# Performance work log

Hardware: AMD Instinct MI355X
Metric: run time of the kernel (lower is better)

## Reference

```python
import jax, jax.numpy as jnp
import numpy as np

EPS = 1e-5

def _conv1x1(x, w, b):
    # x: [B,C,...], w: [O,C], b: [O]
    y = jnp.einsum('oc,bc...->bo...', w, x)
    return y + b.reshape((1, -1) + (1,) * (x.ndim - 2))

def _bn(x, g, be, m, v):
    # inference-mode BatchNorm with running stats (PyTorch eps=1e-5)
    s = (1, -1) + (1,) * (x.ndim - 2)
    return (x - m.reshape(s)) * (g.reshape(s) / jnp.sqrt(v.reshape(s) + EPS)) + be.reshape(s)

def _patches3x3(x):
    # F.unfold(kernel=3, pad=1, stride=1, dil=1): [B,C,H,W] -> [B,C,9,H,W], row-major kernel order
    B, C, H, W = x.shape
    xp = jnp.pad(x, ((0, 0), (0, 0), (1, 1), (1, 1)))
    return jnp.stack([xp[:, :, ky:ky + H, kx:kx + W] for ky in range(3) for kx in range(3)], axis=2)

def setup_inputs() -> dict:
    key = jax.random.key(0)
    ks = jax.random.split(key, 40)
    B, Cin, H, W = 4, 16, 192, 192
    Cm = 64  # mlp[-1]
    d = {}
    d['x'] = jax.random.normal(ks[0], (B, Cin, H, W), jnp.float32)
    d['group_mask'] = jnp.ones((B, 1, H, W), jnp.float32)
    d['group_xyz'] = jax.random.normal(ks[1], (B, 3, 9, H, W), jnp.float32)
    def bnp(k, c):
        k1, k2, k3, k4 = jax.random.split(k, 4)
        return (1.0 + 0.1 * jax.random.normal(k1, (c,)), 0.1 * jax.random.normal(k2, (c,)),
                0.1 * jax.random.normal(k3, (c,)), 0.5 + jax.random.uniform(k4, (c,)))
    d['w0'] = 0.1 * jax.random.normal(ks[2], (Cm, Cin)); d['b0'] = 0.01 * jax.random.normal(ks[3], (Cm,))
    d['g0'], d['beta0'], d['m0'], d['v0'] = bnp(ks[4], Cm)
    wn_dims = [(8, 3), (8, 8), (16, 8)]
    for i, (o, c) in enumerate(wn_dims):
        d[f'wn_w{i}'] = 0.3 * jax.random.normal(ks[5 + 3 * i], (o, c))
        d[f'wn_b{i}'] = 0.01 * jax.random.normal(ks[6 + 3 * i], (o,))
        d[f'wn_g{i}'], d[f'wn_beta{i}'], d[f'wn_m{i}'], d[f'wn_v{i}'] = bnp(ks[7 + 3 * i], o)
    d['lw'] = 0.05 * jax.random.normal(ks[20], (Cm, 16 * Cm)); d['lb'] = 0.01 * jax.random.normal(ks[21], (Cm,))
    d['lg'], d['lbeta'], d['lm'], d['lv'] = bnp(ks[22], Cm)
    return d

def reference(x, group_mask, group_xyz,
              w0, b0, g0, beta0, m0, v0,
              wn_w0, wn_b0, wn_g0, wn_beta0, wn_m0, wn_v0,
              wn_w1, wn_b1, wn_g1, wn_beta1, wn_m1, wn_v1,
              wn_w2, wn_b2, wn_g2, wn_beta2, wn_m2, wn_v2,
              lw, lb, lg, lbeta, lm, lv):
    # mlp_convs chain (single layer here)
    x = jax.nn.relu(_bn(_conv1x1(x, w0, b0), g0, beta0, m0, v0))  # [B,Cm,H,W]
    B, _, N, H, W = group_xyz.shape
    # WeightNet on local coords: [B,3,N,H*W] -> [B,16,N,H*W]
    gz = group_xyz.reshape(B, 3, N, H * W)
    for w, b, g, be, m, v in ((wn_w0, wn_b0, wn_g0, wn_beta0, wn_m0, wn_v0),
                              (wn_w1, wn_b1, wn_g1, wn_beta1, wn_m1, wn_v1),
                              (wn_w2, wn_b2, wn_g2, wn_beta2, wn_m2, wn_v2)):
        gz = jax.nn.relu(_bn(_conv1x1(gz, w, b), g, be, m, v))
    gz = gz.reshape(B, 16, N, H, W)
    p = _patches3x3(x)  # [B,Cm,9,H,W]
    C = p.shape[1]
    # per-pixel matmul: [B,H,W,C,9] @ [B,H,W,9,16] -> [B,H,W,C,16]
    out = jnp.einsum('bckhw,bokhw->bhwco', p, gz)
    out = out.reshape(B, H, W, C * 16).transpose(0, 3, 1, 2)  # [B,16*Cm,H,W]
    return jax.nn.relu(_bn(_conv1x1(out, lw, lb), lg, lbeta, lm, lv))
```

## Files before the change

### kernel.cpp

```cpp
#include <hip/hip_runtime.h>
#include <hip/hip_bf16.h>

#define HH 192
#define WW 192
#define HWPROD (192*192)
#define EPSBN 1e-5f

typedef _Float16 f16x8 __attribute__((ext_vector_type(8)));
typedef _Float16 f16x4 __attribute__((ext_vector_type(4)));
typedef _Float16 f16x2 __attribute__((ext_vector_type(2)));
typedef float f32x4 __attribute__((ext_vector_type(4)));

__global__ __launch_bounds__(256) void prep_conv0_k(
                       const float* __restrict__ w0, const float* __restrict__ b0,
                       const float* __restrict__ g0, const float* __restrict__ beta0,
                       const float* __restrict__ m0, const float* __restrict__ v0,
                       const float* __restrict__ wnw0, const float* __restrict__ wnb0,
                       const float* __restrict__ wng0, const float* __restrict__ wnbe0,
                       const float* __restrict__ wnm0, const float* __restrict__ wnv0,
                       const float* __restrict__ wnw1, const float* __restrict__ wnb1,
                       const float* __restrict__ wng1, const float* __restrict__ wnbe1,
                       const float* __restrict__ wnm1, const float* __restrict__ wnv1,
                       const float* __restrict__ wnw2, const float* __restrict__ wnb2,
                       const float* __restrict__ wng2, const float* __restrict__ wnbe2,
                       const float* __restrict__ wnm2, const float* __restrict__ wnv2,
                       const float* __restrict__ lw, const float* __restrict__ lb,
                       const float* __restrict__ lg, const float* __restrict__ lbeta,
                       const float* __restrict__ lm, const float* __restrict__ lv,
                       const float* __restrict__ x,
                       _Float16* __restrict__ x1L,
                       _Float16* __restrict__ whF,
                       float* __restrict__ lbf,
                       float* __restrict__ wnP)
{
    const int tid = threadIdx.x;

    if (blockIdx.x >= 576) {
        int idx = (blockIdx.x - 576) * 256 + tid;
        if (idx < 65536) {
            int j    = idx & 7;
            int lane = (idx >> 3) & 63;
            int kg   = (idx >> 9) & 31;
            int nt   = idx >> 14;
            int k = kg * 32 + ((lane >> 4) & 3) * 8 + j;
            int n = nt * 16 + (lane & 15);
            float s = lg[n] * rsqrtf(lv[n] + EPSBN);
            whF[idx] = (_Float16)(lw[n * 1024 + k] * s);
        } else if (idx < 65600) {
            int j = idx - 65536;
            float s = lg[j] * rsqrtf(lv[j] + EPSBN);
            lbf[j] = (lb[j] - lm[j]) * s + lbeta[j];
        } else if (idx < 65848) {
            int t = idx - 65600;
            if (t < 24)       { int o = t / 3;           float s = wng0[o] * rsqrtf(wnv0[o] + EPSBN); wnP[t] = wnw0[t] * s; }
            else if (t < 32)  { int o = t - 24;          float s = wng0[o] * rsqrtf(wnv0[o] + EPSBN); wnP[t] = (wnb0[o] - wnm0[o]) * s + wnbe0[o]; }
            else if (t < 96)  { int t2 = t - 32;  int o = t2 >> 3; float s = wng1[o] * rsqrtf(wnv1[o] + EPSBN); wnP[t] = wnw1[t2] * s; }
            else if (t < 104) { int o = t - 96;          float s = wng1[o] * rsqrtf(wnv1[o] + EPSBN); wnP[t] = (wnb1[o] - wnm1[o]) * s + wnbe1[o]; }
            else if (t < 232) { int t2 = t - 104; int o = t2 >> 3; float s = wng2[o] * rsqrtf(wnv2[o] + EPSBN); wnP[t] = wnw2[t2] * s; }
            else if (t < 248) { int o = t - 232;         float s = wng2[o] * rsqrtf(wnv2[o] + EPSBN); wnP[t] = (wnb2[o] - wnm2[o]) * s + wnbe2[o]; }
        }
        return;
    }

    __shared__ float wSt[16][64];
    __shared__ float bS[64];
    for (int t = tid; t < 1024; t += 256) {
        int o = t >> 4, ci = t & 15;
        float s = g0[o] * rsqrtf(v0[o] + EPSBN);
        wSt[ci][o] = w0[t] * s;
    }
    if (tid < 64) {
        float s = g0[tid] * rsqrtf(v0[tid] + EPSBN);
        bS[tid] = (b0[tid] - m0[tid]) * s + beta0[tid];
    }
    __syncthreads();

    const int pix = blockIdx.x * 256 + tid;
    const int b = pix / HWPROD;
    const int p = pix - b * HWPROD;

    float xv[16];
#pragma unroll
    for (int cin = 0; cin < 16; cin++)
        xv[cin] = x[((size_t)b * 16 + cin) * HWPROD + p];

    _Float16* outp = x1L + (size_t)pix * 64;
#pragma unroll
    for (int co = 0; co < 64; co += 4) {
        f32x4 a = { bS[co], bS[co + 1], bS[co + 2], bS[co + 3] };
#pragma unroll
        for (int cin = 0; cin < 16; cin++) {
            float xc = xv[cin];
            a.x += wSt[cin][co + 0] * xc;
            a.y += wSt[cin][co + 1] * xc;
            a.z += wSt[cin][co + 2] * xc;
            a.w += wSt[cin][co + 3] * xc;
        }
        a.x = fmaxf(a.x, 0.f); a.y = fmaxf(a.y, 0.f);
        a.z = fmaxf(a.z, 0.f); a.w = fmaxf(a.w, 0.f);
        *(f16x4*)(outp + co) = __builtin_convertvector(a, f16x4);
    }
}

__global__ __launch_bounds__(512, 4) void pconv_main_k(const float* __restrict__ gxyz,
                                                       const _Float16* __restrict__ x1L,
                                                       const _Float16* __restrict__ whF,
                                                       const float* __restrict__ lbf,
                                                       const float* __restrict__ wnP,
                                                       float* __restrict__ out)
{
    __shared__ __align__(16) char smem[58496];
    f16x2*    xtP = reinterpret_cast<f16x2*>(smem);
    _Float16* A0  = reinterpret_cast<_Float16*>(smem + 25728);
    _Float16* A1  = reinterpret_cast<_Float16*>(smem + 42112);
    _Float16* gzF = reinterpret_cast<_Float16*>(smem + 25728);
    float*    Cb  = reinterpret_cast<float*>(smem);

    const int tid = threadIdx.x;
    const int bid = blockIdx.x;
    const int b   = bid / (HH * 3);
    const int rem = bid % (HH * 3);
    const int h   = rem / 3;
    const int wc0 = (rem % 3) * 64;

    for (int q = tid; q < 1584; q += 512) {
        int c8   = q & 7;
        int colr = q >> 3;
        int col  = colr % 66;
        int r    = colr / 66;
        int hr = h + r - 1;
        int wc = wc0 + col - 1;
        union { f16x8 v; f16x2 p[4]; } U;
        U.v = f16x8{};
        if (hr >= 0 && hr < HH && wc >= 0 && wc < WW) {
            U.v = *(const f16x8*)(x1L + (((size_t)b * HH + hr) * WW + wc) * 64 + c8 * 8);
        }
#pragma unroll
        for (int i = 0; i < 4; i++)
            xtP[(c8 * 4 + i) * 201 + colr] = U.p[i];
    }

    for (int u = tid; u < 576; u += 512) {
        int pixu = u & 63, tap = u >> 6;
        size_t base = ((size_t)(b * 3) * 9 + tap) * HWPROD + (size_t)h * WW + wc0 + pixu;
        float z0 = gxyz[base];
        float z1 = gxyz[base + (size_t)9 * HWPROD];
        float z2 = gxyz[base + (size_t)18 * HWPROD];
        float h0[8], h1[8];
#pragma unroll
        for (int o = 0; o < 8; o++) {
            float a = wnP[24 + o] + wnP[o * 3 + 0] * z0 + wnP[o * 3 + 1] * z1 + wnP[o * 3 + 2] * z2;
            h0[o] = fmaxf(a, 0.f);
        }
#pragma unroll
        for (int o = 0; o < 8; o++) {
            float a = wnP[96 + o];
#pragma unroll
            for (int c = 0; c < 8; c++) a += wnP[32 + o * 8 + c] * h0[c];
            h1[o] = fmaxf(a, 0.f);
        }
        float g[16];
#pragma unroll
        for (int o = 0; o < 16; o++) {
            float a = wnP[232 + o];
#pragma unroll
            for (int c = 0; c < 8; c++) a += wnP[104 + o * 8 + c] * h1[c];
            g[o] = fmaxf(a, 0.f);
        }
        f16x8 lo, hi;
#pragma unroll
        for (int o = 0; o < 8; o++) { lo[o] = (_Float16)g[o]; hi[o] = (_Float16)g[o + 8]; }
        *(f16x8*)&gzF[pixu * 152 + tap * 16]     = lo;
        *(f16x8*)&gzF[pixu * 152 + tap * 16 + 8] = hi;
    }
    __syncthreads();

    const int pix = tid & 63;
    const int u8  = tid >> 6;
    const int oh  = u8 & 1;
    const int cp  = u8 >> 1;
    const int lane = tid & 63;
    const int wv   = tid >> 6;
    const int nt   = wv & 3;
    const int mt2  = wv >> 2;

    f16x2 gq2[9][4];
#pragma unroll
    for (int t = 0; t < 9; t++) {
        union { f16x8 v; f16x2 h[4]; } G;
        G.v = *(const f16x8*)&gzF[pix * 152 + t * 16 + oh * 8];
#pragma unroll
        for (int d = 0; d < 4; d++) gq2[t][d] = G.h[d];
    }
    __syncthreads();

    const int mt = pix >> 4;

    auto phase1 = [&](int cc, _Float16* Ab) {
        union { f16x2 h2[4]; f16x8 v; } av0, av1;
#pragma unroll
        for (int d = 0; d < 4; d++) { av0.h2[d] = f16x2{0, 0}; av1.h2[d] = f16x2{0, 0}; }
        const f16x2* xrow = xtP + (cc * 4 + cp) * 201 + pix;
#pragma unroll
        for (int ky = 0; ky < 3; ky++) {
#pragma unroll
            for (int kx = 0; kx < 3; kx++) {
                const int t = ky * 3 + kx;
                f16x2 xq = xrow[ky * 66 + kx];
                f16x2 xb0 = __builtin_shufflevector(xq, xq, 0, 0);
                f16x2 xb1 = __builtin_shufflevector(xq, xq, 1, 1);
#pragma unroll
                for (int d = 0; d < 4; d++) {
                    av0.h2[d] = __builtin_elementwise_fma(xb0, gq2[t][d], av0.h2[d]);
                    av1.h2[d] = __builtin_elementwise_fma(xb1, gq2[t][d], av1.h2[d]);
                }
            }
        }
        const int row = cp * 4 + mt;
        *(f16x8*)&Ab[(row * 64 + (pix & 15) + 16 * oh) * 8]       = av0.v;
        *(f16x8*)&Ab[(row * 64 + (pix & 15) + 16 * (2 + oh)) * 8] = av1.v;
    };

    const f16x8* whF8 = (const f16x8*)whF;
    f32x4 facc[2];
    facc[0] = f32x4{0.f, 0.f, 0.f, 0.f};
    facc[1] = f32x4{0.f, 0.f, 0.f, 0.f};

    phase1(0, A0);
    __syncthreads();

#pragma unroll 2
    for (int cc = 0; cc < 8; cc++) {
        const _Float16* Ac = (cc & 1) ? A1 : A0;
#pragma unroll
        for (int kb = 0; kb < 4; kb++) {
            const int kg = cc * 4 + kb;
            f16x8 a0 = *(const f16x8*)&Ac[((kb * 4 + 2 * mt2) * 64 + lane) * 8];
            f16x8 a1 = *(const f16x8*)&Ac[((kb * 4 + 2 * mt2 + 1) * 64 + lane) * 8];
            f16x8 wh = whF8[((nt * 32 + kg) << 6) + lane];
            facc[0] = __builtin_amdgcn_mfma_f32_16x16x32_f16(a0, wh, facc[0], 0, 0, 0);
            facc[1] = __builtin_amdgcn_mfma_f32_16x16x32_f16(a1, wh, facc[1], 0, 0, 0);
        }
        if (cc < 7) phase1(cc + 1, (cc & 1) ? A0 : A1);
        __syncthreads();
    }

    {
        const int n = nt * 16 + (lane & 15);
        const float bias = lbf[n];
#pragma unroll
        for (int m = 0; m < 2; m++) {
            const int pixm = (2 * mt2 + m) * 16 + (lane >> 4) * 4;
#pragma unroll
            for (int r = 0; r < 4; r++)
                Cb[n * 67 + pixm + r] = fmaxf(facc[m][r] + bias, 0.f);
        }
    }
    __syncthreads();
    {
        const int pixq = tid & 63, jq = tid >> 6;
        size_t ob = ((size_t)b * 64 + jq * 8) * HWPROD + (size_t)h * WW + wc0 + pixq;
#pragma unroll
        for (int i = 0; i < 8; i++) {
            out[ob + (size_t)i * HWPROD] = Cb[(jq * 8 + i) * 67 + pixq];
        }
    }
}

extern "C" void kernel_launch(void* const* d_in, const int* in_sizes, int n_in,
                              void* d_out, int out_size, void* d_ws, size_t ws_size,
                              hipStream_t stream) {
    const float* x    = (const float*)d_in[0];
    const float* gxyz = (const float*)d_in[2];

    char* ws = (char*)d_ws;
    _Float16* x1L = (_Float16*)ws;
    _Float16* whF = x1L + 9437184;
    float* lbf = (float*)(whF + 65536);
    float* wnP = lbf + 64;

    prep_conv0_k<<<838, 256, 0, stream>>>(
        (const float*)d_in[3],  (const float*)d_in[4],  (const float*)d_in[5],
        (const float*)d_in[6],  (const float*)d_in[7],  (const float*)d_in[8],
        (const float*)d_in[9],  (const float*)d_in[10], (const float*)d_in[11],
        (const float*)d_in[12], (const float*)d_in[13], (const float*)d_in[14],
        (const float*)d_in[15], (const float*)d_in[16], (const float*)d_in[17],
        (const float*)d_in[18], (const float*)d_in[19], (const float*)d_in[20],
        (const float*)d_in[21], (const float*)d_in[22], (const float*)d_in[23],
        (const float*)d_in[24], (const float*)d_in[25], (const float*)d_in[26],
        (const float*)d_in[27], (const float*)d_in[28], (const float*)d_in[29],
        (const float*)d_in[30], (const float*)d_in[31], (const float*)d_in[32],
        x, x1L, whF, lbf, wnP);

    pconv_main_k<<<4 * HH * 3, 512, 0, stream>>>(gxyz, x1L, whF, lbf, wnP,
                                                 (float*)d_out);
}
```

Before: 221.4 us.

## Halve A-tile double buffers to raise occupancy from 4 to 6 blocks

Each phase1 step now builds half as many channels: one scalar channel per thread instead of an f16x2 pair. The K loop therefore runs 16 half-chunks of 2 MFMA k-blocks instead of 8 chunks of 4. This shrinks each A staging buffer by half, which cuts LDS to 45184 bytes, and the launch bounds are raised to 6 blocks per CU so more waves can hide latency. In exchange there are twice as many __syncthreads barriers. It also adds scalar half loads from LDS and lowers the per-thread ILP inside phase1.

```diff
diff --git a/kernel.cpp b/kernel.cpp
--- a/kernel.cpp
+++ b/kernel.cpp
@@ -102,17 +102,17 @@
     }
 }
 
-__global__ __launch_bounds__(512, 4) void pconv_main_k(const float* __restrict__ gxyz,
+__global__ __launch_bounds__(512, 6) void pconv_main_k(const float* __restrict__ gxyz,
                                                        const _Float16* __restrict__ x1L,
                                                        const _Float16* __restrict__ whF,
                                                        const float* __restrict__ lbf,
                                                        const float* __restrict__ wnP,
                                                        float* __restrict__ out)
 {
-    __shared__ __align__(16) char smem[58496];
+    __shared__ __align__(16) char smem[45184];
     f16x2*    xtP = reinterpret_cast<f16x2*>(smem);
     _Float16* A0  = reinterpret_cast<_Float16*>(smem + 25728);
-    _Float16* A1  = reinterpret_cast<_Float16*>(smem + 42112);
+    _Float16* A1  = reinterpret_cast<_Float16*>(smem + 33920);
     _Float16* gzF = reinterpret_cast<_Float16*>(smem + 25728);
     float*    Cb  = reinterpret_cast<float*>(smem);
 
@@ -178,7 +178,7 @@
     const int pix = tid & 63;
     const int u8  = tid >> 6;
     const int oh  = u8 & 1;
-    const int cp  = u8 >> 1;
+    const int cw  = u8 >> 1;
     const int lane = tid & 63;
     const int wv   = tid >> 6;
     const int nt   = wv & 3;
@@ -195,30 +195,27 @@
     __syncthreads();
 
     const int mt = pix >> 4;
-
-    auto phase1 = [&](int cc, _Float16* Ab) {
-        union { f16x2 h2[4]; f16x8 v; } av0, av1;
-#pragma unroll
-        for (int d = 0; d < 4; d++) { av0.h2[d] = f16x2{0, 0}; av1.h2[d] = f16x2{0, 0}; }
-        const f16x2* xrow = xtP + (cc * 4 + cp) * 201 + pix;
+    const _Float16* xtH = reinterpret_cast<const _Float16*>(smem);
+
+    auto phase1 = [&](int hc, _Float16* Ab) {
+        union { f16x2 h2[4]; f16x8 v; } av;
+#pragma unroll
+        for (int d = 0; d < 4; d++) av.h2[d] = f16x2{0, 0};
+        const _Float16* xrow = xtH + (size_t)((hc * 2 + (cw >> 1)) * 201 + pix) * 2 + (cw & 1);
 #pragma unroll
         for (int ky = 0; ky < 3; ky++) {
 #pragma unroll
             for (int kx = 0; kx < 3; kx++) {
                 const int t = ky * 3 + kx;
-                f16x2 xq = xrow[ky * 66 + kx];
-                f16x2 xb0 = __builtin_shufflevector(xq, xq, 0, 0);
-                f16x2 xb1 = __builtin_shufflevector(xq, xq, 1, 1);
-#pragma unroll
-                for (int d = 0; d < 4; d++) {
-                    av0.h2[d] = __builtin_elementwise_fma(xb0, gq2[t][d], av0.h2[d]);
-                    av1.h2[d] = __builtin_elementwise_fma(xb1, gq2[t][d], av1.h2[d]);
-                }
+                _Float16 xs = xrow[(ky * 66 + kx) * 2];
+                f16x2 xb = { xs, xs };
+#pragma unroll
+                for (int d = 0; d < 4; d++)
+                    av.h2[d] = __builtin_elementwise_fma(xb, gq2[t][d], av.h2[d]);
             }
         }
-        const int row = cp * 4 + mt;
-        *(f16x8*)&Ab[(row * 64 + (pix & 15) + 16 * oh) * 8]       = av0.v;
-        *(f16x8*)&Ab[(row * 64 + (pix & 15) + 16 * (2 + oh)) * 8] = av1.v;
+        const int row = (cw >> 1) * 4 + mt;
+        *(f16x8*)&Ab[(row * 64 + (pix & 15) + 16 * ((cw & 1) * 2 + oh)) * 8] = av.v;
     };
 
     const f16x8* whF8 = (const f16x8*)whF;
@@ -230,18 +227,18 @@
     __syncthreads();
 
 #pragma unroll 2
-    for (int cc = 0; cc < 8; cc++) {
-        const _Float16* Ac = (cc & 1) ? A1 : A0;
-#pragma unroll
-        for (int kb = 0; kb < 4; kb++) {
-            const int kg = cc * 4 + kb;
+    for (int hc = 0; hc < 16; hc++) {
+        const _Float16* Ac = (hc & 1) ? A1 : A0;
+#pragma unroll
+        for (int kb = 0; kb < 2; kb++) {
+            const int kg = hc * 2 + kb;
             f16x8 a0 = *(const f16x8*)&Ac[((kb * 4 + 2 * mt2) * 64 + lane) * 8];
             f16x8 a1 = *(const f16x8*)&Ac[((kb * 4 + 2 * mt2 + 1) * 64 + lane) * 8];
             f16x8 wh = whF8[((nt * 32 + kg) << 6) + lane];
             facc[0] = __builtin_amdgcn_mfma_f32_16x16x32_f16(a0, wh, facc[0], 0, 0, 0);
             facc[1] = __builtin_amdgcn_mfma_f32_16x16x32_f16(a1, wh, facc[1], 0, 0, 0);
         }
-        if (cc < 7) phase1(cc + 1, (cc & 1) ? A0 : A1);
+        if (hc < 15) phase1(hc + 1, (hc & 1) ? A0 : A1);
         __syncthreads();
     }
 
```

New measurement: 223.2 us. About the same (+0.8%).

## Switch final GEMM to 32x32x16 MFMA with split-K across wave halves

Applied to the files above, without the earlier changes.

The final 1x1 conv GEMM now uses 32x32x16 MFMA tiles instead of pairs of 16x16x32, with the weight pre-layout and A-tile layout reorganized to match. The eight waves split K by alternating channel chunks: half the waves process even chunks and half odd chunks, then combine partial sums through shared memory before bias and ReLU. This aims to cut the number of MFMA issues and LDS/global weight loads per wave. In exchange it adds a shared-memory reduction step and leaves half of the waves idle during each chunk's MFMA phase.

```diff
diff --git a/kernel.cpp b/kernel.cpp
--- a/kernel.cpp
+++ b/kernel.cpp
@@ -10,6 +10,7 @@
 typedef _Float16 f16x4 __attribute__((ext_vector_type(4)));
 typedef _Float16 f16x2 __attribute__((ext_vector_type(2)));
 typedef float f32x4 __attribute__((ext_vector_type(4)));
+typedef float f32x16 __attribute__((ext_vector_type(16)));
 
 __global__ __launch_bounds__(256) void prep_conv0_k(
                        const float* __restrict__ w0, const float* __restrict__ b0,
@@ -40,10 +41,10 @@
         if (idx < 65536) {
             int j    = idx & 7;
             int lane = (idx >> 3) & 63;
-            int kg   = (idx >> 9) & 31;
-            int nt   = idx >> 14;
-            int k = kg * 32 + ((lane >> 4) & 3) * 8 + j;
-            int n = nt * 16 + (lane & 15);
+            int kg   = (idx >> 9) & 63;
+            int nt   = idx >> 15;
+            int k = kg * 16 + ((lane >> 5) & 1) * 8 + j;
+            int n = nt * 32 + (lane & 31);
             float s = lg[n] * rsqrtf(lv[n] + EPSBN);
             whF[idx] = (_Float16)(lw[n * 1024 + k] * s);
         } else if (idx < 65600) {
@@ -115,6 +116,7 @@
     _Float16* A1  = reinterpret_cast<_Float16*>(smem + 42112);
     _Float16* gzF = reinterpret_cast<_Float16*>(smem + 25728);
     float*    Cb  = reinterpret_cast<float*>(smem);
+    float*    Pb  = reinterpret_cast<float*>(smem + 25728);
 
     const int tid = threadIdx.x;
     const int bid = blockIdx.x;
@@ -181,8 +183,9 @@
     const int cp  = u8 >> 1;
     const int lane = tid & 63;
     const int wv   = tid >> 6;
-    const int nt   = wv & 3;
-    const int mt2  = wv >> 2;
+    const int mt32w = wv & 1;
+    const int nt32  = (wv >> 1) & 1;
+    const int kh    = wv >> 2;
 
     f16x2 gq2[9][4];
 #pragma unroll
@@ -194,7 +197,8 @@
     }
     __syncthreads();
 
-    const int mt = pix >> 4;
+    const int mt32p = pix >> 5;
+    const int p31   = pix & 31;
 
     auto phase1 = [&](int cc, _Float16* Ab) {
         union { f16x2 h2[4]; f16x8 v; } av0, av1;
@@ -216,15 +220,15 @@
                 }
             }
         }
-        const int row = cp * 4 + mt;
-        *(f16x8*)&Ab[(row * 64 + (pix & 15) + 16 * oh) * 8]       = av0.v;
-        *(f16x8*)&Ab[(row * 64 + (pix & 15) + 16 * (2 + oh)) * 8] = av1.v;
+        const int u0 = (cp * 4 + mt32p) * 64 + oh * 32 + p31;
+        *(f16x8*)&Ab[u0 * 8]         = av0.v;
+        *(f16x8*)&Ab[(u0 + 128) * 8] = av1.v;
     };
 
     const f16x8* whF8 = (const f16x8*)whF;
-    f32x4 facc[2];
-    facc[0] = f32x4{0.f, 0.f, 0.f, 0.f};
-    facc[1] = f32x4{0.f, 0.f, 0.f, 0.f};
+    f32x16 facc;
+#pragma unroll
+    for (int r = 0; r < 16; r++) facc[r] = 0.f;
 
     phase1(0, A0);
     __syncthreads();
@@ -232,28 +236,34 @@
 #pragma unroll 2
     for (int cc = 0; cc < 8; cc++) {
         const _Float16* Ac = (cc & 1) ? A1 : A0;
-#pragma unroll
-        for (int kb = 0; kb < 4; kb++) {
-            const int kg = cc * 4 + kb;
-            f16x8 a0 = *(const f16x8*)&Ac[((kb * 4 + 2 * mt2) * 64 + lane) * 8];
-            f16x8 a1 = *(const f16x8*)&Ac[((kb * 4 + 2 * mt2 + 1) * 64 + lane) * 8];
-            f16x8 wh = whF8[((nt * 32 + kg) << 6) + lane];
-            facc[0] = __builtin_amdgcn_mfma_f32_16x16x32_f16(a0, wh, facc[0], 0, 0, 0);
-            facc[1] = __builtin_amdgcn_mfma_f32_16x16x32_f16(a1, wh, facc[1], 0, 0, 0);
+        if ((cc & 1) == kh) {
+#pragma unroll
+            for (int kgl = 0; kgl < 8; kgl++) {
+                f16x8 a  = *(const f16x8*)&Ac[(((kgl * 2 + mt32w) * 64) + lane) * 8];
+                f16x8 wh = whF8[(nt32 * 64 + cc * 8 + kgl) * 64 + lane];
+                facc = __builtin_amdgcn_mfma_f32_32x32x16_f16(a, wh, facc, 0, 0, 0);
+            }
         }
         if (cc < 7) phase1(cc + 1, (cc & 1) ? A0 : A1);
         __syncthreads();
     }
 
-    {
-        const int n = nt * 16 + (lane & 15);
+    const int tile = mt32w * 2 + nt32;
+    if (kh == 1) {
+#pragma unroll
+        for (int r = 0; r < 16; r++)
+            Pb[(tile * 16 + r) * 64 + lane] = facc[r];
+    }
+    __syncthreads();
+    if (kh == 0) {
+        const int n = nt32 * 32 + (lane & 31);
         const float bias = lbf[n];
-#pragma unroll
-        for (int m = 0; m < 2; m++) {
-            const int pixm = (2 * mt2 + m) * 16 + (lane >> 4) * 4;
-#pragma unroll
-            for (int r = 0; r < 4; r++)
-                Cb[n * 67 + pixm + r] = fmaxf(facc[m][r] + bias, 0.f);
+        const int rbase = mt32w * 32 + 4 * (lane >> 5);
+#pragma unroll
+        for (int r = 0; r < 16; r++) {
+            float vsum = facc[r] + Pb[(tile * 16 + r) * 64 + lane] + bias;
+            const int pixm = rbase + (r & 3) + 8 * (r >> 2);
+            Cb[n * 67 + pixm] = fmaxf(vsum, 0.f);
         }
     }
     __syncthreads();
```

Measured after the change: 225.2 us. No clear change (+1.7%).
